# Optimization experiments

Measured on AMD Instinct MI355X. Metric: run time of the kernel, lower is better.

Reference implementation:

```python
import jax, jax.numpy as jnp
import numpy as np
from jax import lax

V, E, HD, B, S, T = 50000, 256, 512, 32, 256, 24
H = HD // 2  # per-direction hidden size


def setup_inputs() -> dict:
    key = jax.random.key(0)
    ks = jax.random.split(key, 15)
    def n(k, shape, scale=0.1):
        return jax.random.normal(k, shape, jnp.float32) * scale
    return dict(
        sentence=jax.random.randint(ks[0], (B, S), 0, V),
        embed=n(ks[1], (V, E)),
        Wih_f=n(ks[2], (4 * H, E)), Whh_f=n(ks[3], (4 * H, H)),
        bih_f=n(ks[4], (4 * H,)), bhh_f=n(ks[5], (4 * H,)),
        Wih_b=n(ks[6], (4 * H, E)), Whh_b=n(ks[7], (4 * H, H)),
        bih_b=n(ks[8], (4 * H,)), bhh_b=n(ks[9], (4 * H,)),
        Wout=n(ks[10], (T, HD)), bout=n(ks[11], (T,)),
        transitions=n(ks[12], (T, T), 1.0),
        start_t=n(ks[13], (T,), 1.0),
        stop_t=n(ks[14], (T,), 1.0),
    )


def _lstm_dir(xs, Wih, Whh, bih, bhh, reverse):
    # xs: [S, B, E] -> hs: [S, B, H]; PyTorch gate order i,f,g,o
    bsz, hh = xs.shape[1], Whh.shape[1]
    x_proj = jnp.einsum('sbe,ge->sbg', xs, Wih) + bih + bhh  # [S,B,4H]
    def step(carry, xp):
        h, c = carry
        gates = xp + h @ Whh.T
        i, f, g, o = jnp.split(gates, 4, axis=-1)
        c = jax.nn.sigmoid(f) * c + jax.nn.sigmoid(i) * jnp.tanh(g)
        h = jax.nn.sigmoid(o) * jnp.tanh(c)
        return (h, c), h
    init = (jnp.zeros((bsz, hh), xs.dtype), jnp.zeros((bsz, hh), xs.dtype))
    _, hs = lax.scan(step, init, x_proj, reverse=reverse)
    return hs


def _features(sentence, embed, Wih_f, Whh_f, bih_f, bhh_f,
              Wih_b, Whh_b, bih_b, bhh_b, Wout, bout):
    emb = embed[sentence]                      # [B,S,E]
    xs = jnp.swapaxes(emb, 0, 1)               # [S,B,E]
    hf = _lstm_dir(xs, Wih_f, Whh_f, bih_f, bhh_f, reverse=False)
    hb = _lstm_dir(xs, Wih_b, Whh_b, bih_b, bhh_b, reverse=True)
    hs = jnp.concatenate([hf, hb], axis=-1)    # [S,B,HD]
    return jnp.einsum('sbh,th->sbt', hs, Wout) + bout  # [S,B,T]


def reference(sentence, embed, Wih_f, Whh_f, bih_f, bhh_f,
              Wih_b, Whh_b, bih_b, bhh_b, Wout, bout,
              transitions, start_t, stop_t):
    feats = _features(sentence, embed, Wih_f, Whh_f, bih_f, bhh_f,
                      Wih_b, Whh_b, bih_b, bhh_b, Wout, bout)  # [S,B,T]
    # Viterbi decode (faithful to _viterbi_decode)
    v0 = feats[0] + start_t[None, :]           # [B,T]
    def step(v, feat):
        scores = v[:, :, None] + transitions[None]  # [B, prev T, next T]
        idx = jnp.argmax(scores, axis=1)       # [B,T] best previous tag
        v = jnp.max(scores, axis=1) + feat
        return v, idx
    v, idxs = lax.scan(step, v0, feats[1:])    # idxs: [S-1,B,T]
    last = jnp.argmax(v + stop_t[None, :], axis=1)  # [B]
    def back(tag, idx):
        tag = jnp.take_along_axis(idx, tag[:, None], axis=1)[:, 0]
        return tag, tag
    _, prev_tags = lax.scan(back, last, idxs, reverse=True)  # [S-1,B]
    tags = jnp.concatenate([prev_tags, last[None]], axis=0)  # [S,B]
    return jnp.swapaxes(tags, 0, 1)            # [B,S]
```

## Files before the change

kernel.cpp:

```cpp
#include <hip/hip_runtime.h>
#include <hip/hip_bf16.h>


#define S_LEN 256
#define BATCH 32
#define NTAG  24

typedef unsigned long long ull;

__global__ __launch_bounds__(256) void k_prep(
    const float* __restrict__ WhhF, const float* __restrict__ WhhB,
    float* __restrict__ Wt) {
  int idx = blockIdx.x * 256 + threadIdx.x;
  int dir = idx >> 18;
  int r = idx & 262143;
  int k = r >> 10;
  int jg = r & 1023;
  int j = jg >> 2, g = jg & 3;
  const float* W = dir ? WhhB : WhhF;
  Wt[idx] = W[(size_t)(g * 256 + j) * 256 + k];
}

__global__ __launch_bounds__(256) void k_inproj(
    const int* __restrict__ sent, const float* __restrict__ embed,
    const float* __restrict__ WihF, const float* __restrict__ bihF, const float* __restrict__ bhhF,
    const float* __restrict__ WihB, const float* __restrict__ bihB, const float* __restrict__ bhhB,
    float* __restrict__ xq) {
  int tm = blockIdx.x;
  int tn = blockIdx.y;
  int dir = blockIdx.z;
  const float* Wih = dir ? WihB : WihF;
  const float* bih = dir ? bihB : bihF;
  const float* bhh = dir ? bhhB : bhhF;
  __shared__ float As[64 * 36];
  __shared__ float Bs[64 * 36];
  __shared__ int toks[64];
  int tid = threadIdx.x;
  if (tid < 64) {
    int r = tm * 64 + tid;
    int s = r >> 5, b = r & 31;
    toks[tid] = sent[b * S_LEN + s];
  }
  __syncthreads();
  int mt = tid & 15, nt = tid >> 4;
  float acc[4][4] = {};
  for (int k0 = 0; k0 < 256; k0 += 32) {
    for (int it = 0; it < 2; ++it) {
      int u = it * 256 + tid;
      int row = u >> 3, lf = u & 7;
      float4 av = *(const float4*)&embed[(size_t)toks[row] * 256 + k0 + lf * 4];
      *(float4*)&As[row * 36 + lf * 4] = av;
      int grow = tn * 64 + row;
      float4 wv = *(const float4*)&Wih[(size_t)grow * 256 + k0 + lf * 4];
      *(float4*)&Bs[row * 36 + lf * 4] = wv;
    }
    __syncthreads();
#pragma unroll
    for (int kc = 0; kc < 8; ++kc) {
      float4 a[4], w[4];
#pragma unroll
      for (int i = 0; i < 4; ++i) a[i] = *(const float4*)&As[(mt + 16 * i) * 36 + kc * 4];
#pragma unroll
      for (int j = 0; j < 4; ++j) w[j] = *(const float4*)&Bs[(nt + 16 * j) * 36 + kc * 4];
#pragma unroll
      for (int i = 0; i < 4; ++i)
#pragma unroll
        for (int j = 0; j < 4; ++j)
          acc[i][j] += a[i].x * w[j].x + a[i].y * w[j].y + a[i].z * w[j].z + a[i].w * w[j].w;
    }
    __syncthreads();
  }
#pragma unroll
  for (int i = 0; i < 4; ++i) {
    int r = tm * 64 + mt + 16 * i;
    int s = r >> 5, b = r & 31;
#pragma unroll
    for (int j = 0; j < 4; ++j) {
      int gg = tn * 64 + nt + 16 * j;
      float v = acc[i][j] + bih[gg] + bhh[gg];
      xq[(((size_t)(dir * 32 + b)) * 256 + s) * 1024 + (gg & 255) * 4 + (gg >> 8)] = v;
    }
  }
}

__global__ __launch_bounds__(256, 1) void k_lstm(
    const float* __restrict__ Wt,
    const float* __restrict__ xq,
    ull* __restrict__ hX2,
    float* __restrict__ hsF) {
  int B = blockIdx.x;
  int q = (B >> 3) & 3;
  int gid = (B & 7) | ((B >> 5) << 3);
  int dir = gid >> 5;
  int b = gid & 31;
  int tid = threadIdx.x;
  int w = tid >> 6;
  int l = tid & 63;
  int kbase = w * 64;
  int unit = q * 64 + l;

  __shared__ float red[4][64 * 8];

  float4 wreg[64];
  {
    const float* wp = Wt + ((size_t)dir * 256 + kbase) * 1024 + unit * 4;
#pragma unroll
    for (int kk = 0; kk < 64; ++kk)
      wreg[kk] = *(const float4*)(wp + (size_t)kk * 1024);
  }

  const size_t grp = ((size_t)dir * 32 + b) * 256;
  const size_t PARSZ = (size_t)2 * 32 * 256;
  float c_st = 0.f;

#pragma unroll 1
  for (int t = 0; t < 256; ++t) {
    int s = dir ? (255 - t) : t;
    unsigned tgt = (unsigned)t;

    float4 xv = {0.f, 0.f, 0.f, 0.f};
    if (w == 0)
      xv = *(const float4*)&xq[(((size_t)(dir * 32 + b)) * 256 + s) * 1024 + unit * 4];

    float hval;
    {
      const ull* hp = hX2 + ((size_t)(t & 1) * PARSZ + grp + kbase + l);
      ull a0 = __hip_atomic_load(hp, __ATOMIC_RELAXED, __HIP_MEMORY_SCOPE_AGENT);
      ull a1 = __hip_atomic_load(hp, __ATOMIC_RELAXED, __HIP_MEMORY_SCOPE_AGENT);
      ull good;
      unsigned spins = 0;
      while (true) {
        if (__all((unsigned)(a0 >> 32) == tgt)) { good = a0; break; }
        a0 = __hip_atomic_load(hp, __ATOMIC_RELAXED, __HIP_MEMORY_SCOPE_AGENT);
        if (__all((unsigned)(a1 >> 32) == tgt)) { good = a1; break; }
        a1 = __hip_atomic_load(hp, __ATOMIC_RELAXED, __HIP_MEMORY_SCOPE_AGENT);
        if (++spins > (1u << 18)) { good = a0; break; }
      }
      hval = __uint_as_float((unsigned)good);
    }

    float4 acc = {0.f, 0.f, 0.f, 0.f};
#pragma unroll
    for (int kk = 0; kk < 64; ++kk) {
      float hk = __shfl(hval, kk);
      acc.x += wreg[kk].x * hk;
      acc.y += wreg[kk].y * hk;
      acc.z += wreg[kk].z * hk;
      acc.w += wreg[kk].w * hk;
    }
    *(float4*)&red[w][l * 8] = acc;
    __syncthreads();

    if (w == 0) {
      float4 r0 = *(const float4*)&red[0][l * 8];
      float4 r1 = *(const float4*)&red[1][l * 8];
      float4 r2 = *(const float4*)&red[2][l * 8];
      float4 r3 = *(const float4*)&red[3][l * 8];
      float xi = r0.x + r1.x + r2.x + r3.x + xv.x;
      float xf = r0.y + r1.y + r2.y + r3.y + xv.y;
      float xg = r0.z + r1.z + r2.z + r3.z + xv.z;
      float xo = r0.w + r1.w + r2.w + r3.w + xv.w;
      float si = 1.f / (1.f + __expf(-xi));
      float sf = 1.f / (1.f + __expf(-xf));
      float so = 1.f / (1.f + __expf(-xo));
      float eg = __expf(-2.f * fabsf(xg));
      float tg = __builtin_copysignf((1.f - eg) / (1.f + eg), xg);
      float c = sf * c_st + si * tg;
      c_st = c;
      float ec = __expf(-2.f * fabsf(c));
      float th = __builtin_copysignf((1.f - ec) / (1.f + ec), c);
      float h = so * th;
      ull atom = ((ull)(unsigned)(t + 1) << 32) | (ull)__float_as_uint(h);
      ull* hn = hX2 + ((size_t)((t + 1) & 1) * PARSZ + grp + unit);
      __hip_atomic_store(hn, atom, __ATOMIC_RELAXED, __HIP_MEMORY_SCOPE_AGENT);
      hsF[(((size_t)(dir * 32 + b)) * 256 + s) * 256 + unit] = h;
    }
  }
}

__global__ __launch_bounds__(256) void k_feats(
    const float* __restrict__ hsF, const float* __restrict__ Wout,
    const float* __restrict__ bout, float* __restrict__ feats) {
  int s = blockIdx.x;
  int tid = threadIdx.x;
  __shared__ float Hl[32 * 260];
  __shared__ float Wl[24 * 260];
  float acc[3] = {};
  for (int dir = 0; dir < 2; ++dir) {
    __syncthreads();
    for (int u = tid; u < 8192; u += 256) {
      int b = u >> 8, j = u & 255;
      Hl[b * 260 + j] = hsF[(((size_t)(dir * 32 + b)) * 256 + s) * 256 + j];
    }
    for (int u = tid; u < 24 * 256; u += 256) {
      int t = u >> 8, j = u & 255;
      Wl[t * 260 + j] = Wout[t * 512 + dir * 256 + j];
    }
    __syncthreads();
    int b = tid & 31, th = tid >> 5;
    for (int jc = 0; jc < 64; ++jc) {
      float4 hv = *(const float4*)&Hl[b * 260 + jc * 4];
#pragma unroll
      for (int rep = 0; rep < 3; ++rep) {
        int t = rep * 8 + th;
        float4 wv = *(const float4*)&Wl[t * 260 + jc * 4];
        acc[rep] += hv.x * wv.x + hv.y * wv.y + hv.z * wv.z + hv.w * wv.w;
      }
    }
  }
  int b = tid & 31, th = tid >> 5;
#pragma unroll
  for (int rep = 0; rep < 3; ++rep) {
    int t = rep * 8 + th;
    feats[((size_t)s * 32 + b) * 24 + t] = acc[rep] + bout[t];
  }
}

__global__ __launch_bounds__(64) void k_viterbi(
    const float* __restrict__ feats, const float* __restrict__ trans,
    const float* __restrict__ start_t, const float* __restrict__ stop_t,
    int* __restrict__ out) {
  int b = blockIdx.x;
  int j = threadIdx.x;
  bool act = j < NTAG;
  int j2 = act ? j : 0;
  __shared__ unsigned char idxL[255 * 24];
  __shared__ float sv[32];
  float tr[24];
#pragma unroll
  for (int i = 0; i < 24; ++i) tr[i] = trans[i * 24 + j2];
  float vj = feats[(size_t)b * 24 + j2] + start_t[j2];
  if (!act) vj = -1e30f;
#pragma unroll 1
  for (int s = 1; s < 256; ++s) {
    float m = -1e30f;
    int arg = 0;
#pragma unroll
    for (int i = 0; i < 24; ++i) {
      float vi = __shfl(vj, i);
      float sc = vi + tr[i];
      if (sc > m) { m = sc; arg = i; }
    }
    float fj = feats[((size_t)s * 32 + b) * 24 + j2];
    if (act) {
      idxL[(s - 1) * 24 + j] = (unsigned char)arg;
      vj = m + fj;
    }
  }
  if (act) sv[j] = vj + stop_t[j];
  __syncthreads();
  if (j == 0) {
    float m = sv[0];
    int tag = 0;
    for (int i = 1; i < 24; ++i)
      if (sv[i] > m) { m = sv[i]; tag = i; }
    out[b * 256 + 255] = tag;
    for (int s = 254; s >= 0; --s) {
      tag = idxL[s * 24 + tag];
      out[b * 256 + s] = tag;
    }
  }
}

extern "C" void kernel_launch(void* const* d_in, const int* in_sizes, int n_in,
                              void* d_out, int out_size, void* d_ws, size_t ws_size,
                              hipStream_t stream) {
  const int*   sent   = (const int*)  d_in[0];
  const float* embed  = (const float*)d_in[1];
  const float* WihF   = (const float*)d_in[2];
  const float* WhhF   = (const float*)d_in[3];
  const float* bihF   = (const float*)d_in[4];
  const float* bhhF   = (const float*)d_in[5];
  const float* WihB   = (const float*)d_in[6];
  const float* WhhB   = (const float*)d_in[7];
  const float* bihB   = (const float*)d_in[8];
  const float* bhhB   = (const float*)d_in[9];
  const float* Wout   = (const float*)d_in[10];
  const float* bout   = (const float*)d_in[11];
  const float* trans  = (const float*)d_in[12];
  const float* startt = (const float*)d_in[13];
  const float* stopt  = (const float*)d_in[14];
  int* out = (int*)d_out;

  char* ws = (char*)d_ws;
  size_t off = 0;
  float* xq = (float*)(ws + off);           off += (size_t)2 * 32 * 256 * 1024 * 4;
  size_t off_sync = off;
  ull* hX2 = (ull*)(ws + off);              off += (size_t)2 * 2 * 32 * 256 * 8;
  size_t sync_len = off - off_sync;
  float* hsF = (float*)(ws + off);          off += (size_t)2 * 32 * 256 * 256 * 4;
  float* feats = (float*)(ws + off);        off += (size_t)256 * 32 * 24 * 4;
  float* Wt = (float*)(ws + off);           off += (size_t)2 * 256 * 1024 * 4;

  hipMemsetAsync(ws + off_sync, 0, sync_len, stream);

  k_prep<<<2048, 256, 0, stream>>>(WhhF, WhhB, Wt);
  k_inproj<<<dim3(128, 16, 2), 256, 0, stream>>>(sent, embed, WihF, bihF, bhhF,
                                                 WihB, bihB, bhhB, xq);
  k_lstm<<<256, 256, 0, stream>>>(Wt, xq, hX2, hsF);
  k_feats<<<256, 256, 0, stream>>>(hsF, Wout, bout, feats);
  k_viterbi<<<32, 64, 0, stream>>>(feats, trans, startt, stopt, out);
}
```

Measured before the change: 1.142 ms.

## Interleave two batch rows per LSTM block and enlarge input-projection GEMM tiles

Measured after the change: 1.796 ms. 57.2% more time.

```diff
diff --git a/kernel.cpp b/kernel.cpp
--- a/kernel.cpp
+++ b/kernel.cpp
@@ -32,51 +32,56 @@
   const float* Wih = dir ? WihB : WihF;
   const float* bih = dir ? bihB : bihF;
   const float* bhh = dir ? bhhB : bhhF;
-  __shared__ float As[64 * 36];
-  __shared__ float Bs[64 * 36];
-  __shared__ int toks[64];
+  __shared__ float As[128 * 36];
+  __shared__ float Bs[128 * 36];
+  __shared__ int toks[128];
   int tid = threadIdx.x;
-  if (tid < 64) {
-    int r = tm * 64 + tid;
+  if (tid < 128) {
+    int r = tm * 128 + tid;
     int s = r >> 5, b = r & 31;
     toks[tid] = sent[b * S_LEN + s];
   }
   __syncthreads();
   int mt = tid & 15, nt = tid >> 4;
-  float acc[4][4] = {};
+  float acc[8][8] = {};
   for (int k0 = 0; k0 < 256; k0 += 32) {
-    for (int it = 0; it < 2; ++it) {
+#pragma unroll
+    for (int it = 0; it < 8; ++it) {
       int u = it * 256 + tid;
-      int row = u >> 3, lf = u & 7;
-      float4 av = *(const float4*)&embed[(size_t)toks[row] * 256 + k0 + lf * 4];
-      *(float4*)&As[row * 36 + lf * 4] = av;
-      int grow = tn * 64 + row;
-      float4 wv = *(const float4*)&Wih[(size_t)grow * 256 + k0 + lf * 4];
-      *(float4*)&Bs[row * 36 + lf * 4] = wv;
+      if (u < 1024) {
+        int row = u >> 3, lf = u & 7;
+        *(float4*)&As[row * 36 + lf * 4] =
+            *(const float4*)&embed[(size_t)toks[row] * 256 + k0 + lf * 4];
+      } else {
+        int v2 = u - 1024;
+        int row = v2 >> 3, lf = v2 & 7;
+        *(float4*)&Bs[row * 36 + lf * 4] =
+            *(const float4*)&Wih[(size_t)(tn * 128 + row) * 256 + k0 + lf * 4];
+      }
     }
     __syncthreads();
 #pragma unroll
     for (int kc = 0; kc < 8; ++kc) {
-      float4 a[4], w[4];
-#pragma unroll
-      for (int i = 0; i < 4; ++i) a[i] = *(const float4*)&As[(mt + 16 * i) * 36 + kc * 4];
-#pragma unroll
-      for (int j = 0; j < 4; ++j) w[j] = *(const float4*)&Bs[(nt + 16 * j) * 36 + kc * 4];
-#pragma unroll
-      for (int i = 0; i < 4; ++i)
-#pragma unroll
-        for (int j = 0; j < 4; ++j)
+      float4 a[8], w[8];
+#pragma unroll
+      for (int i = 0; i < 8; ++i) a[i] = *(const float4*)&As[(mt + 16 * i) * 36 + kc * 4];
+#pragma unroll
+      for (int j = 0; j < 8; ++j) w[j] = *(const float4*)&Bs[(nt + 16 * j) * 36 + kc * 4];
+#pragma unroll
+      for (int i = 0; i < 8; ++i)
+#pragma unroll
+        for (int j = 0; j < 8; ++j)
           acc[i][j] += a[i].x * w[j].x + a[i].y * w[j].y + a[i].z * w[j].z + a[i].w * w[j].w;
     }
     __syncthreads();
   }
 #pragma unroll
-  for (int i = 0; i < 4; ++i) {
-    int r = tm * 64 + mt + 16 * i;
+  for (int i = 0; i < 8; ++i) {
+    int r = tm * 128 + mt + 16 * i;
     int s = r >> 5, b = r & 31;
 #pragma unroll
-    for (int j = 0; j < 4; ++j) {
-      int gg = tn * 64 + nt + 16 * j;
+    for (int j = 0; j < 8; ++j) {
+      int gg = tn * 128 + nt + 16 * j;
       float v = acc[i][j] + bih[gg] + bhh[gg];
       xq[(((size_t)(dir * 32 + b)) * 256 + s) * 1024 + (gg & 255) * 4 + (gg >> 8)] = v;
     }
@@ -90,16 +95,20 @@
     float* __restrict__ hsF) {
   int B = blockIdx.x;
   int q = (B >> 3) & 3;
-  int gid = (B & 7) | ((B >> 5) << 3);
-  int dir = gid >> 5;
-  int b = gid & 31;
+  int g = (B & 7) | ((B >> 5) << 3);
+  int dir = g >> 4;
+  int bA = g & 15;
+  int bB = bA + 16;
+  int gidA = dir * 32 + bA;
+  int gidB = dir * 32 + bB;
   int tid = threadIdx.x;
   int w = tid >> 6;
   int l = tid & 63;
   int kbase = w * 64;
   int unit = q * 64 + l;
 
-  __shared__ float red[4][64 * 8];
+  __shared__ float redA[2][4][64 * 8];
+  __shared__ float redB[2][4][64 * 8];
 
   float4 wreg[64];
   {
@@ -109,71 +118,118 @@
       wreg[kk] = *(const float4*)(wp + (size_t)kk * 1024);
   }
 
-  const size_t grp = ((size_t)dir * 32 + b) * 256;
-  const size_t PARSZ = (size_t)2 * 32 * 256;
-  float c_st = 0.f;
+  const size_t PARSZ = (size_t)64 * 256;
+  const size_t grpA = (size_t)gidA * 256;
+  const size_t grpB = (size_t)gidB * 256;
+  float c_A = 0.f, c_B = 0.f;
 
 #pragma unroll 1
   for (int t = 0; t < 256; ++t) {
     int s = dir ? (255 - t) : t;
+    int par = t & 1;
     unsigned tgt = (unsigned)t;
 
-    float4 xv = {0.f, 0.f, 0.f, 0.f};
-    if (w == 0)
-      xv = *(const float4*)&xq[(((size_t)(dir * 32 + b)) * 256 + s) * 1024 + unit * 4];
+    float4 xvA = {0.f, 0.f, 0.f, 0.f}, xvB = xvA;
+    if (w == 0) {
+      xvA = *(const float4*)&xq[((size_t)gidA * 256 + s) * 1024 + unit * 4];
+      xvB = *(const float4*)&xq[((size_t)gidB * 256 + s) * 1024 + unit * 4];
+    }
 
     float hval;
     {
-      const ull* hp = hX2 + ((size_t)(t & 1) * PARSZ + grp + kbase + l);
-      ull a0 = __hip_atomic_load(hp, __ATOMIC_RELAXED, __HIP_MEMORY_SCOPE_AGENT);
-      ull a1 = __hip_atomic_load(hp, __ATOMIC_RELAXED, __HIP_MEMORY_SCOPE_AGENT);
-      ull good;
+      const ull* hp = hX2 + ((size_t)par * PARSZ + grpA + kbase + l);
+      ull a = __hip_atomic_load(hp, __ATOMIC_RELAXED, __HIP_MEMORY_SCOPE_AGENT);
       unsigned spins = 0;
-      while (true) {
-        if (__all((unsigned)(a0 >> 32) == tgt)) { good = a0; break; }
-        a0 = __hip_atomic_load(hp, __ATOMIC_RELAXED, __HIP_MEMORY_SCOPE_AGENT);
-        if (__all((unsigned)(a1 >> 32) == tgt)) { good = a1; break; }
-        a1 = __hip_atomic_load(hp, __ATOMIC_RELAXED, __HIP_MEMORY_SCOPE_AGENT);
-        if (++spins > (1u << 18)) { good = a0; break; }
-      }
-      hval = __uint_as_float((unsigned)good);
-    }
-
-    float4 acc = {0.f, 0.f, 0.f, 0.f};
-#pragma unroll
-    for (int kk = 0; kk < 64; ++kk) {
-      float hk = __shfl(hval, kk);
-      acc.x += wreg[kk].x * hk;
-      acc.y += wreg[kk].y * hk;
-      acc.z += wreg[kk].z * hk;
-      acc.w += wreg[kk].w * hk;
-    }
-    *(float4*)&red[w][l * 8] = acc;
-    __syncthreads();
-
+      while (!__all((unsigned)(a >> 32) == tgt)) {
+        a = __hip_atomic_load(hp, __ATOMIC_RELAXED, __HIP_MEMORY_SCOPE_AGENT);
+        if (++spins > (1u << 18)) break;
+      }
+      hval = __uint_as_float((unsigned)a);
+    }
+    {
+      float4 acc = {0.f, 0.f, 0.f, 0.f};
+#pragma unroll
+      for (int kk = 0; kk < 64; ++kk) {
+        float hk = __shfl(hval, kk);
+        acc.x += wreg[kk].x * hk;
+        acc.y += wreg[kk].y * hk;
+        acc.z += wreg[kk].z * hk;
+        acc.w += wreg[kk].w * hk;
+      }
+      *(float4*)&redA[par][w][l * 8] = acc;
+    }
+    __syncthreads();
     if (w == 0) {
-      float4 r0 = *(const float4*)&red[0][l * 8];
-      float4 r1 = *(const float4*)&red[1][l * 8];
-      float4 r2 = *(const float4*)&red[2][l * 8];
-      float4 r3 = *(const float4*)&red[3][l * 8];
-      float xi = r0.x + r1.x + r2.x + r3.x + xv.x;
-      float xf = r0.y + r1.y + r2.y + r3.y + xv.y;
-      float xg = r0.z + r1.z + r2.z + r3.z + xv.z;
-      float xo = r0.w + r1.w + r2.w + r3.w + xv.w;
+      float4 r0 = *(const float4*)&redA[par][0][l * 8];
+      float4 r1 = *(const float4*)&redA[par][1][l * 8];
+      float4 r2 = *(const float4*)&redA[par][2][l * 8];
+      float4 r3 = *(const float4*)&redA[par][3][l * 8];
+      float xi = r0.x + r1.x + r2.x + r3.x + xvA.x;
+      float xf = r0.y + r1.y + r2.y + r3.y + xvA.y;
+      float xg = r0.z + r1.z + r2.z + r3.z + xvA.z;
+      float xo = r0.w + r1.w + r2.w + r3.w + xvA.w;
       float si = 1.f / (1.f + __expf(-xi));
       float sf = 1.f / (1.f + __expf(-xf));
       float so = 1.f / (1.f + __expf(-xo));
       float eg = __expf(-2.f * fabsf(xg));
       float tg = __builtin_copysignf((1.f - eg) / (1.f + eg), xg);
-      float c = sf * c_st + si * tg;
-      c_st = c;
+      float c = sf * c_A + si * tg;
+      c_A = c;
       float ec = __expf(-2.f * fabsf(c));
       float th = __builtin_copysignf((1.f - ec) / (1.f + ec), c);
       float h = so * th;
       ull atom = ((ull)(unsigned)(t + 1) << 32) | (ull)__float_as_uint(h);
-      ull* hn = hX2 + ((size_t)((t + 1) & 1) * PARSZ + grp + unit);
-      __hip_atomic_store(hn, atom, __ATOMIC_RELAXED, __HIP_MEMORY_SCOPE_AGENT);
-      hsF[(((size_t)(dir * 32 + b)) * 256 + s) * 256 + unit] = h;
+      __hip_atomic_store(hX2 + ((size_t)(par ^ 1) * PARSZ + grpA + unit), atom,
+                         __ATOMIC_RELAXED, __HIP_MEMORY_SCOPE_AGENT);
+      hsF[((size_t)gidA * 256 + s) * 256 + unit] = h;
+    }
+
+    {
+      const ull* hp = hX2 + ((size_t)par * PARSZ + grpB + kbase + l);
+      ull a = __hip_atomic_load(hp, __ATOMIC_RELAXED, __HIP_MEMORY_SCOPE_AGENT);
+      unsigned spins = 0;
+      while (!__all((unsigned)(a >> 32) == tgt)) {
+        a = __hip_atomic_load(hp, __ATOMIC_RELAXED, __HIP_MEMORY_SCOPE_AGENT);
+        if (++spins > (1u << 18)) break;
+      }
+      hval = __uint_as_float((unsigned)a);
+    }
+    {
+      float4 acc = {0.f, 0.f, 0.f, 0.f};
+#pragma unroll
+      for (int kk = 0; kk < 64; ++kk) {
+        float hk = __shfl(hval, kk);
+        acc.x += wreg[kk].x * hk;
+        acc.y += wreg[kk].y * hk;
+        acc.z += wreg[kk].z * hk;
+        acc.w += wreg[kk].w * hk;
+      }
+      *(float4*)&redB[par][w][l * 8] = acc;
+    }
+    __syncthreads();
+    if (w == 0) {
+      float4 r0 = *(const float4*)&redB[par][0][l * 8];
+      float4 r1 = *(const float4*)&redB[par][1][l * 8];
+      float4 r2 = *(const float4*)&redB[par][2][l * 8];
+      float4 r3 = *(const float4*)&redB[par][3][l * 8];
+      float xi = r0.x + r1.x + r2.x + r3.x + xvB.x;
+      float xf = r0.y + r1.y + r2.y + r3.y + xvB.y;
+      float xg = r0.z + r1.z + r2.z + r3.z + xvB.z;
+      float xo = r0.w + r1.w + r2.w + r3.w + xvB.w;
+      float si = 1.f / (1.f + __expf(-xi));
+      float sf = 1.f / (1.f + __expf(-xf));
+      float so = 1.f / (1.f + __expf(-xo));
+      float eg = __expf(-2.f * fabsf(xg));
+      float tg = __builtin_copysignf((1.f - eg) / (1.f + eg), xg);
+      float c = sf * c_B + si * tg;
+      c_B = c;
+      float ec = __expf(-2.f * fabsf(c));
+      float th = __builtin_copysignf((1.f - ec) / (1.f + ec), c);
+      float h = so * th;
+      ull atom = ((ull)(unsigned)(t + 1) << 32) | (ull)__float_as_uint(h);
+      __hip_atomic_store(hX2 + ((size_t)(par ^ 1) * PARSZ + grpB + unit), atom,
+                         __ATOMIC_RELAXED, __HIP_MEMORY_SCOPE_AGENT);
+      hsF[((size_t)gidB * 256 + s) * 256 + unit] = h;
     }
   }
 }
@@ -286,7 +342,7 @@
   size_t off = 0;
   float* xq = (float*)(ws + off);           off += (size_t)2 * 32 * 256 * 1024 * 4;
   size_t off_sync = off;
-  ull* hX2 = (ull*)(ws + off);              off += (size_t)2 * 2 * 32 * 256 * 8;
+  ull* hX2 = (ull*)(ws + off);              off += (size_t)2 * 64 * 256 * 8;
   size_t sync_len = off - off_sync;
   float* hsF = (float*)(ws + off);          off += (size_t)2 * 32 * 256 * 256 * 4;
   float* feats = (float*)(ws + off);        off += (size_t)256 * 32 * 24 * 4;
@@ -295,9 +351,9 @@
   hipMemsetAsync(ws + off_sync, 0, sync_len, stream);
 
   k_prep<<<2048, 256, 0, stream>>>(WhhF, WhhB, Wt);
-  k_inproj<<<dim3(128, 16, 2), 256, 0, stream>>>(sent, embed, WihF, bihF, bhhF,
-                                                 WihB, bihB, bhhB, xq);
-  k_lstm<<<256, 256, 0, stream>>>(Wt, xq, hX2, hsF);
+  k_inproj<<<dim3(64, 8, 2), 256, 0, stream>>>(sent, embed, WihF, bihF, bhhF,
+                                               WihB, bihB, bhhB, xq);
+  k_lstm<<<128, 256, 0, stream>>>(Wt, xq, hX2, hsF);
   k_feats<<<256, 256, 0, stream>>>(hsF, Wout, bout, feats);
   k_viterbi<<<32, 64, 0, stream>>>(feats, trans, startt, stopt, out);
 }
```
